# Kernel tuning notes

Measured on AMD Instinct MI355X. Metric: run time of the kernel, lower is better.

The kernel has to match this reference:

```python
import jax, jax.numpy as jnp
import numpy as np

K = 16

def _local_cov(points):
    # points: [B, N, 3]. FoldingNet-style local covariance feature.
    xx = jnp.sum(points * points, axis=-1)                       # [B,N]
    inner = jnp.einsum('bnd,bmd->bnm', points, points)           # [B,N,N]
    pd = -xx[:, :, None] + 2.0 * inner - xx[:, None, :]          # negative sq dist
    _, idx = jax.lax.top_k(pd, K)                                # [B,N,K] nearest first (self at 0)
    n0 = jnp.take_along_axis(points, idx[:, :, 0][:, :, None], axis=1)  # [B,N,3]
    n1 = jnp.take_along_axis(points, idx[:, :, 1][:, :, None], axis=1)  # [B,N,3]
    cov = n0[..., :, None] * n1[..., None, :]                    # [B,N,3,3] outer product
    B, N = points.shape[0], points.shape[1]
    return jnp.concatenate([points, cov.reshape(B, N, 9)], axis=-1)     # [B,N,12]

def _stage(x, w1, b1, wr, br, w2, b2):
    h = jax.nn.relu(x @ w1 + b1)
    h = jax.nn.relu(h + (h @ wr + br))   # ResidualLinearLayer then ReLU
    return h @ w2 + b2                   # [B,N,1]

def setup_inputs() -> dict:
    key = jax.random.key(0)
    ks = jax.random.split(key, 16)
    B, N, F = 8, 4096, 512
    s = 0.02
    d = {
        'latent': jax.random.normal(ks[0], (B, N, F), jnp.float32),
        'reconstructed_points': jax.random.normal(ks[1], (B, 3, N), jnp.float32),
        's1_w1': jax.random.normal(ks[2], (F + 12, F), jnp.float32) * s,
        's1_b1': jnp.zeros((F,), jnp.float32),
        's1_wr': jax.random.normal(ks[3], (F, F), jnp.float32) * s,
        's1_br': jnp.zeros((F,), jnp.float32),
        's1_w2': jax.random.normal(ks[4], (F, 1), jnp.float32) * s,
        's1_b2': jnp.zeros((1,), jnp.float32),
        's2_w1': jax.random.normal(ks[5], (F + 1, F), jnp.float32) * s,
        's2_b1': jnp.zeros((F,), jnp.float32),
        's2_wr': jax.random.normal(ks[6], (F, F), jnp.float32) * s,
        's2_br': jnp.zeros((F,), jnp.float32),
        's2_w2': jax.random.normal(ks[7], (F, 1), jnp.float32) * s,
        's2_b2': jnp.zeros((1,), jnp.float32),
        's3_w1': jax.random.normal(ks[8], (F + 1, F), jnp.float32) * s,
        's3_b1': jnp.zeros((F,), jnp.float32),
        's3_wr': jax.random.normal(ks[9], (F, F), jnp.float32) * s,
        's3_br': jnp.zeros((F,), jnp.float32),
        's3_w2': jax.random.normal(ks[10], (F, 1), jnp.float32) * s,
        's3_b2': jnp.zeros((1,), jnp.float32),
    }
    return d

def reference(latent, reconstructed_points,
              s1_w1, s1_b1, s1_wr, s1_br, s1_w2, s1_b2,
              s2_w1, s2_b1, s2_wr, s2_br, s2_w2, s2_b2,
              s3_w1, s3_b1, s3_wr, s3_br, s3_w2, s3_b2):
    pts = jnp.transpose(reconstructed_points, (0, 2, 1))   # [B,N,3]
    local = _local_cov(pts)                                 # [B,N,12]
    f1 = jnp.concatenate([latent, local], axis=-1)
    std1 = _stage(f1, s1_w1, s1_b1, s1_wr, s1_br, s1_w2, s1_b2)
    f2 = jnp.concatenate([latent, std1], axis=-1)
    std2 = std1 + _stage(f2, s2_w1, s2_b1, s2_wr, s2_br, s2_w2, s2_b2)
    f3 = jnp.concatenate([latent, std2], axis=-1)
    std3 = std2 + _stage(f3, s3_w1, s3_b1, s3_wr, s3_br, s3_w2, s3_b2)
    return std3   # [B,N,1]
```

## Files before the change

kernel.cpp:

```cpp
#include <hip/hip_runtime.h>

typedef __bf16 bf16x8 __attribute__((ext_vector_type(8)));
typedef float f32x16 __attribute__((ext_vector_type(16)));

__device__ __forceinline__ unsigned short f2bf(float f) {
  unsigned u = __float_as_uint(f);
  u += 0x7FFFu + ((u >> 16) & 1u);
  return (unsigned short)(u >> 16);
}

__device__ __forceinline__ void gload_lds16(const void* g, void* l) {
  __builtin_amdgcn_global_load_lds((const __attribute__((address_space(1))) void*)g,
                                   (__attribute__((address_space(3))) void*)l,
                                   16, 0, 0);
}

#define NPTS 4096
#define LDX 576

__global__ __launch_bounds__(256) void convw6_kernel(
    const float* w0, const float* w1, const float* w2,
    const float* r0, const float* r1, const float* r2,
    unsigned short* d0, unsigned short* d1, unsigned short* d2,
    unsigned short* e0, unsigned short* e1, unsigned short* e2) {
  int z = blockIdx.z;
  const float* src; unsigned short* dst; int Ksrc, Kpad, addI;
  switch (z) {
    case 0: src = w0; dst = d0; Ksrc = 524; Kpad = 576; addI = 0; break;
    case 1: src = w1; dst = d1; Ksrc = 513; Kpad = 576; addI = 0; break;
    case 2: src = w2; dst = d2; Ksrc = 513; Kpad = 576; addI = 0; break;
    case 3: src = r0; dst = e0; Ksrc = 512; Kpad = 512; addI = 1; break;
    case 4: src = r1; dst = e1; Ksrc = 512; Kpad = 512; addI = 1; break;
    default: src = r2; dst = e2; Ksrc = 512; Kpad = 512; addI = 1; break;
  }
  int k0 = blockIdx.x * 32;
  if (k0 >= Kpad) return;
  __shared__ float tile[32][33];
  int n0 = blockIdx.y * 32;
  int tx = threadIdx.x & 31, ty = threadIdx.x >> 5;
#pragma unroll
  for (int r = 0; r < 32; r += 8) {
    int k = k0 + ty + r, n = n0 + tx;
    tile[ty + r][tx] = (k < Ksrc) ? src[(size_t)k * 512 + n] : 0.f;
  }
  __syncthreads();
#pragma unroll
  for (int r = 0; r < 32; r += 8) {
    int n = n0 + ty + r, k = k0 + tx;
    float v = tile[tx][ty + r];
    if (addI && n == k) v += 1.0f;
    dst[(size_t)n * Kpad + k] = f2bf(v);
  }
}

__global__ __launch_bounds__(256) void conv_latent_kernel(const float* __restrict__ latent,
                                                          unsigned short* __restrict__ X) {
  size_t idx = (size_t)blockIdx.x * 256 + threadIdx.x;
  size_t m = idx >> 7;
  int c4 = (int)(idx & 127) * 4;
  float4 v = *(const float4*)(latent + m * 512 + c4);
  ushort4 o;
  o.x = f2bf(v.x); o.y = f2bf(v.y); o.z = f2bf(v.z); o.w = f2bf(v.w);
  *(ushort4*)(X + m * LDX + c4) = o;
}

__device__ __forceinline__ void merge1(float& v, int& j, int mk) {
  float ov = __shfl_xor(v, mk); int oj = __shfl_xor(j, mk);
  bool take = (ov > v) || (ov == v && oj < j);
  v = take ? ov : v; j = take ? oj : j;
}

__global__ __launch_bounds__(512) void knn_kernel(const float* __restrict__ rp,
                                                  unsigned short* __restrict__ X) {
  __shared__ float4 P[NPTS];
  int b = blockIdx.y;
  const float* base = rp + (size_t)b * 3 * NPTS;
  for (int j = threadIdx.x; j < NPTS; j += 512) {
    float x = base[j], y = base[NPTS + j], z = base[2 * NPTS + j];
    float xx = __fadd_rn(__fadd_rn(__fmul_rn(x, x), __fmul_rn(y, y)), __fmul_rn(z, z));
    P[j] = make_float4(x, y, z, -xx);
  }
  __syncthreads();
  int wave = threadIdx.x >> 6, lane = threadIdx.x & 63;
  int grp = lane >> 4, slice = lane & 15;
  int il0 = wave * 8 + grp * 2;
  int ia = blockIdx.x * 64 + il0;
  int ib = ia + 1;
  float4 pa = P[ia], pb = P[ib];
  float ax = 2.f * pa.x, ay = 2.f * pa.y, az = 2.f * pa.z;
  float bx = 2.f * pb.x, by = 2.f * pb.y, bz = 2.f * pb.z;
  float va = -3.4e38f, vb = -3.4e38f;
  int ta = 0, tb = 0;
  int sta = ((ia & 15) == slice) ? (ia >> 4) : -1;
  int stb = ((ib & 15) == slice) ? (ib >> 4) : -1;
  const float4* pp = P + slice;
#pragma unroll 8
  for (int t = 0; t < NPTS / 16; ++t) {
    float4 pj = pp[t * 16];
    float ea = __builtin_fmaf(ax, pj.x, __builtin_fmaf(ay, pj.y,
               __builtin_fmaf(az, pj.z, pj.w)));
    float eb = __builtin_fmaf(bx, pj.x, __builtin_fmaf(by, pj.y,
               __builtin_fmaf(bz, pj.z, pj.w)));
    ea = (t == sta) ? -3.4e38f : ea;
    eb = (t == stb) ? -3.4e38f : eb;
    bool ca = ea > va; va = ca ? ea : va; ta = ca ? t : ta;
    bool cb = eb > vb; vb = cb ? eb : vb; tb = cb ? t : tb;
  }
  int ja = ta * 16 + slice, jb = tb * 16 + slice;
#pragma unroll
  for (int mk = 1; mk <= 8; mk <<= 1) {
    merge1(va, ja, mk);
    merge1(vb, jb, mk);
  }
  if (slice == 0) {
#pragma unroll
    for (int p = 0; p < 2; ++p) {
      float4 pi = (p == 0) ? pa : pb;
      float4 p1 = P[(p == 0) ? ja : jb];
      size_t row = (size_t)b * NPTS + ia + p;
      unsigned short* xp = X + row * LDX + 512;
      float vals[12] = { pi.x, pi.y, pi.z,
                         pi.x * p1.x, pi.x * p1.y, pi.x * p1.z,
                         pi.y * p1.x, pi.y * p1.y, pi.y * p1.z,
                         pi.z * p1.x, pi.z * p1.y, pi.z * p1.z };
#pragma unroll
      for (int k = 0; k < 12; ++k) xp[k] = f2bf(vals[k]);
#pragma unroll
      for (int k = 12; k < 32; ++k) xp[k] = 0;
    }
  }
}

#define BM 256
#define BN 256
#define BK 64
#define GRP 520
#define MBLK 128
#define LDSU16 (2 * 64 * GRP)

__global__ __launch_bounds__(512) void gemm_relu_kernel(
    const unsigned short* __restrict__ Xb, const unsigned short* __restrict__ Wt,
    const float* __restrict__ bias, unsigned short* __restrict__ H,
    int K, int ldx, int ldw,
    const float* __restrict__ std1, const float* __restrict__ std2,
    const float* __restrict__ w1row) {
  extern __shared__ unsigned short S[];
  const int t = threadIdx.x;
  const int wave = t >> 6, lane = t & 63;
  const int flat = blockIdx.y * gridDim.x + blockIdx.x;
  const int m0 = (flat & (MBLK - 1)) * BM;
  const int n0 = (flat >> 7) * BN;
  const int wm = (wave >> 1) * 64;
  const int wn = (wave & 1) * 128;
  const int srow = lane >> 3;
  const int sslot = (lane & 7) ^ srow;
  const int l31 = lane & 31, hi = lane >> 5;
  const int w7 = l31 & 7, g2 = l31 >> 3;
  const unsigned short* Arow = Xb + (size_t)(m0 + srow) * ldx + sslot * 8;
  const unsigned short* Brow = Wt + (size_t)(n0 + srow) * ldw + sslot * 8;
  f32x16 acc[2][4] = {};
  const int nt = K / BK;
  auto STAGE = [&](int buf, int kt) {
#pragma unroll
    for (int r = 0; r < 4; ++r) {
      int g = wave + r * 8;
      gload_lds16(Arow + (size_t)g * 8 * ldx + kt, S + buf * (64 * GRP) + g * GRP);
    }
#pragma unroll
    for (int r = 0; r < 4; ++r) {
      int g = wave + r * 8;
      gload_lds16(Brow + (size_t)g * 8 * ldw + kt, S + buf * (64 * GRP) + (32 + g) * GRP);
    }
  };
  STAGE(0, 0);
  for (int tt = 0; tt < nt; ++tt) {
    const int cur = tt & 1;
    if (tt + 1 < nt) {
      STAGE(cur ^ 1, (tt + 1) * BK);
      asm volatile("s_waitcnt vmcnt(8)" ::: "memory");
    } else {
      asm volatile("s_waitcnt vmcnt(0)" ::: "memory");
    }
    __builtin_amdgcn_s_barrier();
    asm volatile("" ::: "memory");
    const unsigned short* Sa = S + cur * (64 * GRP);
    const unsigned short* Sb = Sa + 32 * GRP;
#pragma unroll
    for (int ks = 0; ks < 4; ++ks) {
      int qx = (ks * 2 + hi) ^ w7;
      bf16x8 a[2], bb[4];
#pragma unroll
      for (int i = 0; i < 2; ++i)
        a[i] = *(const bf16x8*)(Sa + ((wm >> 3) + i * 4 + g2) * GRP + w7 * 64 + qx * 8);
#pragma unroll
      for (int j = 0; j < 4; ++j)
        bb[j] = *(const bf16x8*)(Sb + ((wn >> 3) + j * 4 + g2) * GRP + w7 * 64 + qx * 8);
#pragma unroll
      for (int i = 0; i < 2; ++i)
#pragma unroll
        for (int j = 0; j < 4; ++j)
          acc[i][j] = __builtin_amdgcn_mfma_f32_32x32x16_bf16(a[i], bb[j], acc[i][j], 0, 0, 0);
    }
    asm volatile("" ::: "memory");
    __builtin_amdgcn_sched_barrier(0);
    __builtin_amdgcn_s_barrier();
    asm volatile("" ::: "memory");
  }
  if (w1row) {
    float wv[4];
#pragma unroll
    for (int j = 0; j < 4; ++j) wv[j] = w1row[n0 + wn + j * 32 + l31];
#pragma unroll
    for (int i = 0; i < 2; ++i) {
#pragma unroll
      for (int rg = 0; rg < 16; ++rg) {
        int row = m0 + wm + i * 32 + (rg & 3) + 8 * (rg >> 2) + 4 * hi;
        float sv = std1[row];
        if (std2) sv += std2[row];
#pragma unroll
        for (int j = 0; j < 4; ++j) acc[i][j][rg] += sv * wv[j];
      }
    }
  }
#pragma unroll
  for (int j = 0; j < 4; ++j) {
    int col = n0 + wn + j * 32 + l31;
    float bv = bias[col];
#pragma unroll
    for (int i = 0; i < 2; ++i) {
#pragma unroll
      for (int rg = 0; rg < 16; ++rg) {
        int row = m0 + wm + i * 32 + (rg & 3) + 8 * (rg >> 2) + 4 * hi;
        float v = acc[i][j][rg] + bv;
        v = v > 0.f ? v : 0.f;
        H[(size_t)row * 512 + col] = f2bf(v);
      }
    }
  }
}

__global__ __launch_bounds__(512) void gemm_res_kernel(
    const unsigned short* __restrict__ H1, const unsigned short* __restrict__ Wt,
    const float* __restrict__ br, const float* __restrict__ w2,
    float* __restrict__ so) {
  extern __shared__ unsigned short S[];
  const int t = threadIdx.x;
  const int wave = t >> 6, lane = t & 63;
  const int flat = blockIdx.y * gridDim.x + blockIdx.x;
  const int m0 = (flat & (MBLK - 1)) * BM;
  const int n0 = (flat >> 7) * BN;
  const int wm = (wave >> 1) * 64;
  const int wn = (wave & 1) * 128;
  const int srow = lane >> 3;
  const int sslot = (lane & 7) ^ srow;
  const int l31 = lane & 31, hi = lane >> 5;
  const int w7 = l31 & 7, g2 = l31 >> 3;
  const unsigned short* Arow = H1 + (size_t)(m0 + srow) * 512 + sslot * 8;
  const unsigned short* Brow = Wt + (size_t)(n0 + srow) * 512 + sslot * 8;
  f32x16 acc[2][4] = {};
  auto STAGE = [&](int buf, int kt) {
#pragma unroll
    for (int r = 0; r < 4; ++r) {
      int g = wave + r * 8;
      gload_lds16(Arow + (size_t)g * 8 * 512 + kt, S + buf * (64 * GRP) + g * GRP);
    }
#pragma unroll
    for (int r = 0; r < 4; ++r) {
      int g = wave + r * 8;
      gload_lds16(Brow + (size_t)g * 8 * 512 + kt, S + buf * (64 * GRP) + (32 + g) * GRP);
    }
  };
  STAGE(0, 0);
  const int nt = 512 / BK;
  for (int tt = 0; tt < nt; ++tt) {
    const int cur = tt & 1;
    if (tt + 1 < nt) {
      STAGE(cur ^ 1, (tt + 1) * BK);
      asm volatile("s_waitcnt vmcnt(8)" ::: "memory");
    } else {
      asm volatile("s_waitcnt vmcnt(0)" ::: "memory");
    }
    __builtin_amdgcn_s_barrier();
    asm volatile("" ::: "memory");
    const unsigned short* Sa = S + cur * (64 * GRP);
    const unsigned short* Sb = Sa + 32 * GRP;
#pragma unroll
    for (int ks = 0; ks < 4; ++ks) {
      int qx = (ks * 2 + hi) ^ w7;
      bf16x8 a[2], bb[4];
#pragma unroll
      for (int i = 0; i < 2; ++i)
        a[i] = *(const bf16x8*)(Sa + ((wm >> 3) + i * 4 + g2) * GRP + w7 * 64 + qx * 8);
#pragma unroll
      for (int j = 0; j < 4; ++j)
        bb[j] = *(const bf16x8*)(Sb + ((wn >> 3) + j * 4 + g2) * GRP + w7 * 64 + qx * 8);
#pragma unroll
      for (int i = 0; i < 2; ++i)
#pragma unroll
        for (int j = 0; j < 4; ++j)
          acc[i][j] = __builtin_amdgcn_mfma_f32_32x32x16_bf16(a[i], bb[j], acc[i][j], 0, 0, 0);
    }
    asm volatile("" ::: "memory");
    __builtin_amdgcn_sched_barrier(0);
    __builtin_amdgcn_s_barrier();
    asm volatile("" ::: "memory");
  }
  float bv[4], wv[4];
#pragma unroll
  for (int j = 0; j < 4; ++j) {
    int col = n0 + wn + j * 32 + l31;
    bv[j] = br[col]; wv[j] = w2[col];
  }
#pragma unroll
  for (int i = 0; i < 2; ++i) {
#pragma unroll
    for (int rg = 0; rg < 16; ++rg) {
      float s = 0.f;
#pragma unroll
      for (int j = 0; j < 4; ++j) {
        float v = acc[i][j][rg] + bv[j];
        v = v > 0.f ? v : 0.f;
        s += v * wv[j];
      }
      s += __shfl_xor(s, 1); s += __shfl_xor(s, 2); s += __shfl_xor(s, 4);
      s += __shfl_xor(s, 8); s += __shfl_xor(s, 16);
      if (l31 == 0) {
        int row = m0 + wm + i * 32 + (rg & 3) + 8 * (rg >> 2) + 4 * hi;
        atomicAdd(&so[row], s);
      }
    }
  }
}

__global__ __launch_bounds__(256) void init_so3_kernel(float* so0, float* so1, float* so2,
                                                       const float* b2_0, const float* b2_1,
                                                       const float* b2_2) {
  int m = blockIdx.x * 256 + threadIdx.x;
  so0[m] = b2_0[0];
  so1[m] = b2_1[0];
  so2[m] = b2_2[0];
}
__global__ __launch_bounds__(256) void finalize_kernel(float* out, const float* so0,
                                                       const float* so1, const float* so2) {
  int m = blockIdx.x * 256 + threadIdx.x;
  out[m] = so0[m] + so1[m] + so2[m];
}

extern "C" void kernel_launch(void* const* d_in, const int* in_sizes, int n_in,
                              void* d_out, int out_size, void* d_ws, size_t ws_size,
                              hipStream_t stream) {
  const int B = 8, N = NPTS, M = B * N;
  const float* latent = (const float*)d_in[0];
  const float* rp = (const float*)d_in[1];
  const float* w1[3] = {(const float*)d_in[2], (const float*)d_in[8], (const float*)d_in[14]};
  const float* b1[3] = {(const float*)d_in[3], (const float*)d_in[9], (const float*)d_in[15]};
  const float* wr[3] = {(const float*)d_in[4], (const float*)d_in[10], (const float*)d_in[16]};
  const float* br[3] = {(const float*)d_in[5], (const float*)d_in[11], (const float*)d_in[17]};
  const float* w2[3] = {(const float*)d_in[6], (const float*)d_in[12], (const float*)d_in[18]};
  const float* b2[3] = {(const float*)d_in[7], (const float*)d_in[13], (const float*)d_in[19]};

  char* ws = (char*)d_ws;
  auto carve = [&](size_t bytes) {
    char* p = ws;
    ws += (bytes + 255) & ~(size_t)255;
    return p;
  };
  unsigned short* X  = (unsigned short*)carve((size_t)M * LDX * 2);
  unsigned short* H1 = (unsigned short*)carve((size_t)M * 512 * 2);
  unsigned short* W1t[3], *Wrt[3];
  for (int s = 0; s < 3; ++s) W1t[s] = (unsigned short*)carve((size_t)512 * LDX * 2);
  for (int s = 0; s < 3; ++s) Wrt[s] = (unsigned short*)carve((size_t)512 * 512 * 2);
  float* so0 = (float*)carve((size_t)M * 4);
  float* so1 = (float*)carve((size_t)M * 4);
  float* so2 = (float*)carve((size_t)M * 4);

  const size_t ldsBytes = (size_t)LDSU16 * 2;

  convw6_kernel<<<dim3(LDX / 32, 16, 6), 256, 0, stream>>>(
      w1[0], w1[1], w1[2], wr[0], wr[1], wr[2],
      W1t[0], W1t[1], W1t[2], Wrt[0], Wrt[1], Wrt[2]);
  conv_latent_kernel<<<(M * 128) / 256, 256, 0, stream>>>(latent, X);
  knn_kernel<<<dim3(N / 64, B), 512, 0, stream>>>(rp, X);
  init_so3_kernel<<<M / 256, 256, 0, stream>>>(so0, so1, so2, b2[0], b2[1], b2[2]);

  float* soArr[3] = {so0, so1, so2};
  for (int s = 0; s < 3; ++s) {
    if (s == 0) {
      gemm_relu_kernel<<<dim3(512 / BN, M / BM), 512, ldsBytes, stream>>>(
          X, W1t[s], b1[s], H1, LDX, LDX, LDX, nullptr, nullptr, nullptr);
    } else {
      gemm_relu_kernel<<<dim3(512 / BN, M / BM), 512, ldsBytes, stream>>>(
          X, W1t[s], b1[s], H1, 512, LDX, LDX,
          so0, (s == 2) ? so1 : nullptr, w1[s] + (size_t)512 * 512);
    }
    gemm_res_kernel<<<dim3(512 / BN, M / BM), 512, ldsBytes, stream>>>(
        H1, Wrt[s], br[s], w2[s], soArr[s]);
  }
  finalize_kernel<<<M / 256, 256, 0, stream>>>((float*)d_out, so0, so1, so2);
}
```

Measured before the change: 358.1 us.

## Batch all three stage first-layer GEMMs into one wide GEMM, apply std rank-1 later

The first-layer weights of all three stages are concatenated so that a single GEMM computes latent@W1 for every stage at once, writing pre-activations into a 1536-wide buffer. The std-dependent rank-1 term, bias and ReLU for stages 2 and 3 are then applied while the residual GEMM loads its A tile, instead of rerunning the 576-wide GEMM per stage. This removes two GEMM passes over X and two launches. In exchange the residual GEMM drops its double-buffered async pipeline for stages 2 and 3 and adds register-side bf16 conversion work, and the pre-activations are rounded to bf16 before the rank-1 add.

```diff
diff --git a/kernel.cpp b/kernel.cpp
--- a/kernel.cpp
+++ b/kernel.cpp
@@ -17,6 +17,13 @@
 
 #define NPTS 4096
 #define LDX 576
+#define LDH 1536
+#define BM 256
+#define BN 256
+#define BK 64
+#define GRP 520
+#define MBLK 128
+#define LDSU16 (2 * 64 * GRP)
 
 __global__ __launch_bounds__(256) void convw6_kernel(
     const float* w0, const float* w1, const float* w2,
@@ -27,8 +34,8 @@
   const float* src; unsigned short* dst; int Ksrc, Kpad, addI;
   switch (z) {
     case 0: src = w0; dst = d0; Ksrc = 524; Kpad = 576; addI = 0; break;
-    case 1: src = w1; dst = d1; Ksrc = 513; Kpad = 576; addI = 0; break;
-    case 2: src = w2; dst = d2; Ksrc = 513; Kpad = 576; addI = 0; break;
+    case 1: src = w1; dst = d1; Ksrc = 512; Kpad = 576; addI = 0; break;
+    case 2: src = w2; dst = d2; Ksrc = 512; Kpad = 576; addI = 0; break;
     case 3: src = r0; dst = e0; Ksrc = 512; Kpad = 512; addI = 1; break;
     case 4: src = r1; dst = e1; Ksrc = 512; Kpad = 512; addI = 1; break;
     default: src = r2; dst = e2; Ksrc = 512; Kpad = 512; addI = 1; break;
@@ -126,50 +133,43 @@
 #pragma unroll
       for (int k = 0; k < 12; ++k) xp[k] = f2bf(vals[k]);
 #pragma unroll
-      for (int k = 12; k < 32; ++k) xp[k] = 0;
-    }
-  }
-}
-
-#define BM 256
-#define BN 256
-#define BK 64
-#define GRP 520
-#define MBLK 128
-#define LDSU16 (2 * 64 * GRP)
-
-__global__ __launch_bounds__(512) void gemm_relu_kernel(
-    const unsigned short* __restrict__ Xb, const unsigned short* __restrict__ Wt,
-    const float* __restrict__ bias, unsigned short* __restrict__ H,
-    int K, int ldx, int ldw,
-    const float* __restrict__ std1, const float* __restrict__ std2,
-    const float* __restrict__ w1row) {
+      for (int k = 12; k < 64; ++k) xp[k] = 0;
+    }
+  }
+}
+
+__global__ __launch_bounds__(512) void gemm_big1(
+    const unsigned short* __restrict__ Xb, const unsigned short* __restrict__ Wcat,
+    const float* __restrict__ b1_0, const float* __restrict__ b1_1,
+    const float* __restrict__ b1_2, unsigned short* __restrict__ H) {
   extern __shared__ unsigned short S[];
   const int t = threadIdx.x;
   const int wave = t >> 6, lane = t & 63;
-  const int flat = blockIdx.y * gridDim.x + blockIdx.x;
+  const int flat = blockIdx.x;
   const int m0 = (flat & (MBLK - 1)) * BM;
   const int n0 = (flat >> 7) * BN;
+  const int stage = n0 >> 9;
+  const float* bias = (stage == 0) ? b1_0 : ((stage == 1) ? b1_1 : b1_2);
   const int wm = (wave >> 1) * 64;
   const int wn = (wave & 1) * 128;
   const int srow = lane >> 3;
   const int sslot = (lane & 7) ^ srow;
   const int l31 = lane & 31, hi = lane >> 5;
   const int w7 = l31 & 7, g2 = l31 >> 3;
-  const unsigned short* Arow = Xb + (size_t)(m0 + srow) * ldx + sslot * 8;
-  const unsigned short* Brow = Wt + (size_t)(n0 + srow) * ldw + sslot * 8;
+  const unsigned short* Arow = Xb + (size_t)(m0 + srow) * LDX + sslot * 8;
+  const unsigned short* Brow = Wcat + (size_t)(n0 + srow) * LDX + sslot * 8;
   f32x16 acc[2][4] = {};
-  const int nt = K / BK;
+  const int nt = LDX / BK;
   auto STAGE = [&](int buf, int kt) {
 #pragma unroll
     for (int r = 0; r < 4; ++r) {
       int g = wave + r * 8;
-      gload_lds16(Arow + (size_t)g * 8 * ldx + kt, S + buf * (64 * GRP) + g * GRP);
+      gload_lds16(Arow + (size_t)g * 8 * LDX + kt, S + buf * (64 * GRP) + g * GRP);
     }
 #pragma unroll
     for (int r = 0; r < 4; ++r) {
       int g = wave + r * 8;
-      gload_lds16(Brow + (size_t)g * 8 * ldw + kt, S + buf * (64 * GRP) + (32 + g) * GRP);
+      gload_lds16(Brow + (size_t)g * 8 * LDX + kt, S + buf * (64 * GRP) + (32 + g) * GRP);
     }
   };
   STAGE(0, 0);
@@ -206,47 +206,35 @@
     __builtin_amdgcn_s_barrier();
     asm volatile("" ::: "memory");
   }
-  if (w1row) {
-    float wv[4];
-#pragma unroll
-    for (int j = 0; j < 4; ++j) wv[j] = w1row[n0 + wn + j * 32 + l31];
-#pragma unroll
-    for (int i = 0; i < 2; ++i) {
-#pragma unroll
-      for (int rg = 0; rg < 16; ++rg) {
-        int row = m0 + wm + i * 32 + (rg & 3) + 8 * (rg >> 2) + 4 * hi;
-        float sv = std1[row];
-        if (std2) sv += std2[row];
-#pragma unroll
-        for (int j = 0; j < 4; ++j) acc[i][j][rg] += sv * wv[j];
-      }
-    }
-  }
 #pragma unroll
   for (int j = 0; j < 4; ++j) {
     int col = n0 + wn + j * 32 + l31;
-    float bv = bias[col];
+    float bv = bias[col & 511];
 #pragma unroll
     for (int i = 0; i < 2; ++i) {
 #pragma unroll
       for (int rg = 0; rg < 16; ++rg) {
         int row = m0 + wm + i * 32 + (rg & 3) + 8 * (rg >> 2) + 4 * hi;
         float v = acc[i][j][rg] + bv;
-        v = v > 0.f ? v : 0.f;
-        H[(size_t)row * 512 + col] = f2bf(v);
-      }
-    }
-  }
-}
-
-__global__ __launch_bounds__(512) void gemm_res_kernel(
-    const unsigned short* __restrict__ H1, const unsigned short* __restrict__ Wt,
+        if (stage == 0) v = v > 0.f ? v : 0.f;
+        H[(size_t)row * LDH + col] = f2bf(v);
+      }
+    }
+  }
+}
+
+__global__ __launch_bounds__(512) void gemm_res2(
+    const unsigned short* __restrict__ Hpre, int soff,
+    const unsigned short* __restrict__ Wt,
     const float* __restrict__ br, const float* __restrict__ w2,
-    float* __restrict__ so) {
-  extern __shared__ unsigned short S[];
+    float* __restrict__ so,
+    const float* __restrict__ std1, const float* __restrict__ std2,
+    const float* __restrict__ w1row) {
+  __shared__ unsigned short As[32 * GRP];
+  __shared__ unsigned short Bs[32 * GRP];
   const int t = threadIdx.x;
   const int wave = t >> 6, lane = t & 63;
-  const int flat = blockIdx.y * gridDim.x + blockIdx.x;
+  const int flat = blockIdx.x;
   const int m0 = (flat & (MBLK - 1)) * BM;
   const int n0 = (flat >> 7) * BN;
   const int wm = (wave >> 1) * 64;
@@ -255,55 +243,67 @@
   const int sslot = (lane & 7) ^ srow;
   const int l31 = lane & 31, hi = lane >> 5;
   const int w7 = l31 & 7, g2 = l31 >> 3;
-  const unsigned short* Arow = H1 + (size_t)(m0 + srow) * 512 + sslot * 8;
   const unsigned short* Brow = Wt + (size_t)(n0 + srow) * 512 + sslot * 8;
+  size_t grow[4]; float sr[4];
+#pragma unroll
+  for (int r = 0; r < 4; ++r) {
+    int row = m0 + (wave + r * 8) * 8 + srow;
+    grow[r] = (size_t)row * LDH + soff + sslot * 8;
+    sr[r] = (std1 != nullptr) ? (std1[row] + (std2 ? std2[row] : 0.f)) : 0.f;
+  }
   f32x16 acc[2][4] = {};
-  auto STAGE = [&](int buf, int kt) {
+  for (int kt = 0; kt < 512; kt += BK) {
 #pragma unroll
     for (int r = 0; r < 4; ++r) {
       int g = wave + r * 8;
-      gload_lds16(Arow + (size_t)g * 8 * 512 + kt, S + buf * (64 * GRP) + g * GRP);
-    }
-#pragma unroll
-    for (int r = 0; r < 4; ++r) {
-      int g = wave + r * 8;
-      gload_lds16(Brow + (size_t)g * 8 * 512 + kt, S + buf * (64 * GRP) + (32 + g) * GRP);
-    }
-  };
-  STAGE(0, 0);
-  const int nt = 512 / BK;
-  for (int tt = 0; tt < nt; ++tt) {
-    const int cur = tt & 1;
-    if (tt + 1 < nt) {
-      STAGE(cur ^ 1, (tt + 1) * BK);
-      asm volatile("s_waitcnt vmcnt(8)" ::: "memory");
+      gload_lds16(Brow + (size_t)g * 8 * 512 + kt, Bs + g * GRP);
+    }
+    if (std1 == nullptr) {
+#pragma unroll
+      for (int r = 0; r < 4; ++r) {
+        int g = wave + r * 8;
+        gload_lds16(Hpre + grow[r] + kt, As + g * GRP);
+      }
     } else {
-      asm volatile("s_waitcnt vmcnt(0)" ::: "memory");
-    }
-    __builtin_amdgcn_s_barrier();
-    asm volatile("" ::: "memory");
-    const unsigned short* Sa = S + cur * (64 * GRP);
-    const unsigned short* Sb = Sa + 32 * GRP;
+      float4 wlo = *(const float4*)(w1row + kt + sslot * 8);
+      float4 whi = *(const float4*)(w1row + kt + sslot * 8 + 4);
+      float wv[8] = {wlo.x, wlo.y, wlo.z, wlo.w, whi.x, whi.y, whi.z, whi.w};
+#pragma unroll
+      for (int r = 0; r < 4; ++r) {
+        uint4 av = *(const uint4*)(Hpre + grow[r] + kt);
+        unsigned uu[4] = {av.x, av.y, av.z, av.w};
+        unsigned o[4];
+#pragma unroll
+        for (int q = 0; q < 4; ++q) {
+          float f0 = __uint_as_float(uu[q] << 16);
+          float f1 = __uint_as_float(uu[q] & 0xffff0000u);
+          f0 = __builtin_fmaf(sr[r], wv[2 * q], f0);
+          f1 = __builtin_fmaf(sr[r], wv[2 * q + 1], f1);
+          f0 = fmaxf(f0, 0.f);
+          f1 = fmaxf(f1, 0.f);
+          o[q] = (unsigned)f2bf(f0) | ((unsigned)f2bf(f1) << 16);
+        }
+        *(uint4*)(As + (wave + r * 8) * GRP + lane * 8) = make_uint4(o[0], o[1], o[2], o[3]);
+      }
+    }
+    __syncthreads();
 #pragma unroll
     for (int ks = 0; ks < 4; ++ks) {
       int qx = (ks * 2 + hi) ^ w7;
       bf16x8 a[2], bb[4];
 #pragma unroll
       for (int i = 0; i < 2; ++i)
-        a[i] = *(const bf16x8*)(Sa + ((wm >> 3) + i * 4 + g2) * GRP + w7 * 64 + qx * 8);
+        a[i] = *(const bf16x8*)(As + ((wm >> 3) + i * 4 + g2) * GRP + w7 * 64 + qx * 8);
 #pragma unroll
       for (int j = 0; j < 4; ++j)
-        bb[j] = *(const bf16x8*)(Sb + ((wn >> 3) + j * 4 + g2) * GRP + w7 * 64 + qx * 8);
+        bb[j] = *(const bf16x8*)(Bs + ((wn >> 3) + j * 4 + g2) * GRP + w7 * 64 + qx * 8);
 #pragma unroll
       for (int i = 0; i < 2; ++i)
 #pragma unroll
         for (int j = 0; j < 4; ++j)
           acc[i][j] = __builtin_amdgcn_mfma_f32_32x32x16_bf16(a[i], bb[j], acc[i][j], 0, 0, 0);
     }
-    asm volatile("" ::: "memory");
-    __builtin_amdgcn_sched_barrier(0);
-    __builtin_amdgcn_s_barrier();
-    asm volatile("" ::: "memory");
+    __syncthreads();
   }
   float bv[4], wv[4];
 #pragma unroll
@@ -365,36 +365,35 @@
     ws += (bytes + 255) & ~(size_t)255;
     return p;
   };
-  unsigned short* X  = (unsigned short*)carve((size_t)M * LDX * 2);
-  unsigned short* H1 = (unsigned short*)carve((size_t)M * 512 * 2);
-  unsigned short* W1t[3], *Wrt[3];
-  for (int s = 0; s < 3; ++s) W1t[s] = (unsigned short*)carve((size_t)512 * LDX * 2);
+  unsigned short* X    = (unsigned short*)carve((size_t)M * LDX * 2);
+  unsigned short* Hpre = (unsigned short*)carve((size_t)M * LDH * 2);
+  unsigned short* Wcat = (unsigned short*)carve((size_t)1536 * LDX * 2);
+  unsigned short* Wrt[3];
   for (int s = 0; s < 3; ++s) Wrt[s] = (unsigned short*)carve((size_t)512 * 512 * 2);
   float* so0 = (float*)carve((size_t)M * 4);
   float* so1 = (float*)carve((size_t)M * 4);
   float* so2 = (float*)carve((size_t)M * 4);
 
-  const size_t ldsBytes = (size_t)LDSU16 * 2;
+  const size_t ldsBig = (size_t)LDSU16 * 2;
 
   convw6_kernel<<<dim3(LDX / 32, 16, 6), 256, 0, stream>>>(
       w1[0], w1[1], w1[2], wr[0], wr[1], wr[2],
-      W1t[0], W1t[1], W1t[2], Wrt[0], Wrt[1], Wrt[2]);
+      Wcat, Wcat + (size_t)512 * LDX, Wcat + (size_t)1024 * LDX,
+      Wrt[0], Wrt[1], Wrt[2]);
   conv_latent_kernel<<<(M * 128) / 256, 256, 0, stream>>>(latent, X);
   knn_kernel<<<dim3(N / 64, B), 512, 0, stream>>>(rp, X);
   init_so3_kernel<<<M / 256, 256, 0, stream>>>(so0, so1, so2, b2[0], b2[1], b2[2]);
 
+  gemm_big1<<<dim3((M / BM) * (LDH / BN)), 512, ldsBig, stream>>>(
+      X, Wcat, b1[0], b1[1], b1[2], Hpre);
+
   float* soArr[3] = {so0, so1, so2};
   for (int s = 0; s < 3; ++s) {
-    if (s == 0) {
-      gemm_relu_kernel<<<dim3(512 / BN, M / BM), 512, ldsBytes, stream>>>(
-          X, W1t[s], b1[s], H1, LDX, LDX, LDX, nullptr, nullptr, nullptr);
-    } else {
-      gemm_relu_kernel<<<dim3(512 / BN, M / BM), 512, ldsBytes, stream>>>(
-          X, W1t[s], b1[s], H1, 512, LDX, LDX,
-          so0, (s == 2) ? so1 : nullptr, w1[s] + (size_t)512 * 512);
-    }
-    gemm_res_kernel<<<dim3(512 / BN, M / BM), 512, ldsBytes, stream>>>(
-        H1, Wrt[s], br[s], w2[s], soArr[s]);
+    gemm_res2<<<dim3((M / BM) * (512 / BN)), 512, 0, stream>>>(
+        Hpre, s * 512, Wrt[s], br[s], w2[s], soArr[s],
+        (s == 0) ? nullptr : so0,
+        (s == 2) ? so1 : nullptr,
+        (s == 0) ? nullptr : (w1[s] + (size_t)512 * 512));
   }
   finalize_kernel<<<M / 256, 256, 0, stream>>>((float*)d_out, so0, so1, so2);
 }
```

Measured after the change: 324.6 us. 1.1x faster.
